# Optimization experiments

Hardware: AMD Instinct MI355X
Metric: run time of the kernel (lower is better)

## Reference

```python
import jax, jax.numpy as jnp
import numpy as np

T, B, D, H = 4096, 4, 1024, 8
EPS = 1e-5


def _ln(z, g, b):
    m = jnp.mean(z, axis=-1, keepdims=True)
    v = jnp.mean((z - m) ** 2, axis=-1, keepdims=True)
    return (z - m) * jax.lax.rsqrt(v + EPS) * g + b


def setup_inputs() -> dict:
    key = jax.random.key(0)
    ks = jax.random.split(key, 8)
    s = 0.02
    return {
        "x": jax.random.normal(ks[0], (T, B, D), dtype=jnp.float32),
        "norm_w": jnp.ones((D,), jnp.float32),
        "norm_b": jnp.zeros((D,), jnp.float32),
        "tnorm_w": jnp.ones((D,), jnp.float32),
        "tnorm_b": jnp.zeros((D,), jnp.float32),
        "Wq": jax.random.normal(ks[1], (D, D), jnp.float32) * s,
        "bq": jnp.zeros((D,), jnp.float32),
        "Wk": jax.random.normal(ks[2], (D, D), jnp.float32) * s,
        "bk": jnp.zeros((D,), jnp.float32),
        "Wv": jax.random.normal(ks[3], (D, D), jnp.float32) * s,
        "bv": jnp.zeros((D,), jnp.float32),
    }


def reference(x, norm_w, norm_b, tnorm_w, tnorm_b, Wq, bq, Wk, bk, Wv, bv):
    # x: (T, B, D) -> (B, T, D), matching torch x.permute(1, 0, 2)
    xb = jnp.transpose(x, (1, 0, 2))
    b, t, d = xb.shape
    hd = d // H
    xn = _ln(xb, norm_w, norm_b)          # query branch norm
    xtn = _ln(xb, tnorm_w, tnorm_b)       # key/value branch norm (text_norm applied to x)
    q = (xn @ Wq.T + bq).reshape(b, t, H, hd)
    k = (xtn @ Wk.T + bk).reshape(b, t, H, hd)
    v = (xtn @ Wv.T + bv).reshape(b, t, H, hd)
    q = jax.nn.softmax(q, axis=-1)        # softmax over head-dim
    k = jax.nn.softmax(k, axis=1)         # softmax over time
    # kv state: (B, H, hd, hd)
    att = jnp.einsum('bthd,bthl->bhdl', k, v)
    y = jnp.einsum('bthd,bhdl->bthl', q, att).reshape(b, t, d)
    return y  # original forward returns y directly (proj_out/dropout unused)
```

## Files before the change

kernel.cpp:

```cpp
#include <hip/hip_runtime.h>
#include <cstdint>

#define T_LEN 4096
#define BATCH 4
#define DIM   1024
#define NH    8
#define HDIM  128
#define ROWS  16384

typedef __bf16 bf16x8 __attribute__((ext_vector_type(8)));
typedef float  f32x4  __attribute__((ext_vector_type(4)));

__device__ __forceinline__ unsigned short f2bf(float f) {
  union { float f; unsigned u; } a; a.f = f;
  unsigned u = a.u;
  u += 0x7fff + ((u >> 16) & 1);
  return (unsigned short)(u >> 16);
}
__device__ __forceinline__ float bf2f(unsigned short h) {
  union { unsigned u; float f; } a; a.u = ((unsigned)h) << 16;
  return a.f;
}

__device__ __forceinline__ void gld_lds16(const unsigned short* g, unsigned short* l) {
  __builtin_amdgcn_global_load_lds(
      (const __attribute__((address_space(1))) unsigned int*)g,
      (__attribute__((address_space(3))) unsigned int*)l, 16, 0, 0);
}

__global__ __launch_bounds__(256) void ln_kernel(
    const float* __restrict__ x, const float* __restrict__ nw, const float* __restrict__ nb,
    const float* __restrict__ tw, const float* __restrict__ tb,
    unsigned short* __restrict__ xn, unsigned short* __restrict__ xtn) {
  int row = blockIdx.x;
  int t = row >> 2, b = row & 3;
  int tid = threadIdx.x;
  const float4 v = ((const float4*)(x + (size_t)row * DIM))[tid];
  float s  = v.x + v.y + v.z + v.w;
  float s2 = v.x*v.x + v.y*v.y + v.z*v.z + v.w*v.w;
#pragma unroll
  for (int o = 32; o; o >>= 1) { s += __shfl_xor(s, o); s2 += __shfl_xor(s2, o); }
  __shared__ float red[8];
  int wv = tid >> 6;
  if ((tid & 63) == 0) { red[wv] = s; red[4 + wv] = s2; }
  __syncthreads();
  s  = red[0] + red[1] + red[2] + red[3];
  s2 = red[4] + red[5] + red[6] + red[7];
  float mean = s * (1.0f / DIM);
  float var  = s2 * (1.0f / DIM) - mean * mean;
  float rstd = rsqrtf(var + 1e-5f);
  size_t orow = ((size_t)b * T_LEN + t) * DIM;
  int c0 = tid * 4;
  float xv[4] = {v.x, v.y, v.z, v.w};
  union { unsigned short u[4]; uint2 d; } o1, o2;
#pragma unroll
  for (int j = 0; j < 4; ++j) {
    int c = c0 + j;
    float xh = (xv[j] - mean) * rstd;
    o1.u[j] = f2bf(xh * nw[c] + nb[c]);
    o2.u[j] = f2bf(xh * tw[c] + tb[c]);
  }
  *(uint2*)(xn  + orow + c0) = o1.d;
  *(uint2*)(xtn + orow + c0) = o2.d;
}

__global__ __launch_bounds__(256) void wconv(
    const float* __restrict__ Wq, const float* __restrict__ Wk, const float* __restrict__ Wv,
    unsigned short* __restrict__ out) {
  int i4 = blockIdx.x * 256 + threadIdx.x;
  int w = i4 >> 18;
  const float* src = (w == 0) ? Wq : (w == 1 ? Wk : Wv);
  float4 v = ((const float4*)src)[i4 & 262143];
  union { unsigned short u[4]; uint2 d; } o;
  o.u[0] = f2bf(v.x); o.u[1] = f2bf(v.y); o.u[2] = f2bf(v.z); o.u[3] = f2bf(v.w);
  ((uint2*)out)[i4] = o.d;
}

template<int MODE>
__global__ __launch_bounds__(256) void qkv_gemm(
    const unsigned short* __restrict__ A, const unsigned short* __restrict__ W,
    const float* __restrict__ bias,
    unsigned short* __restrict__ outp, float* __restrict__ Zk) {
  int m0t = blockIdx.x * 128;
  int n0 = blockIdx.y * 128;
  __shared__ __align__(16) unsigned short smem[128 * 136];
  unsigned short* As = smem;
  unsigned short* Bs = smem + 8192;
  int tid = threadIdx.x;
  int wave = tid >> 6, lane = tid & 63;
  int wm = (wave >> 1) * 64, wn = (wave & 1) * 64;
  int l16 = lane & 15, kq = lane >> 4;
  int swz = l16 & 7;

  int srow = tid >> 3;
  int skk  = (((tid & 7) ^ ((tid >> 3) & 7)) * 8);
  const unsigned short* Ag = A + (size_t)(m0t + srow) * DIM + skk;
  const unsigned short* Wg = W + (size_t)(n0 + srow) * DIM + skk;
  unsigned short* Al = As + wave * 512;
  unsigned short* Bl = Bs + wave * 512;

  f32x4 acc[4][4] = {};

  for (int kt = 0; kt < DIM; kt += 64) {
#pragma unroll
    for (int p = 0; p < 4; ++p) {
      gld_lds16(Ag + (size_t)(p * 32) * DIM + kt, Al + p * 2048);
      gld_lds16(Wg + (size_t)(p * 32) * DIM + kt, Bl + p * 2048);
    }
    __syncthreads();
#pragma unroll
    for (int ks4 = 0; ks4 < 2; ++ks4) {
      int coff = (((kq + ks4 * 4) ^ swz) * 8);
      bf16x8 fa[4], fb[4];
#pragma unroll
      for (int i = 0; i < 4; ++i) {
        fa[i] = *(const bf16x8*)(As + (wm + i * 16 + l16) * 64 + coff);
        fb[i] = *(const bf16x8*)(Bs + (wn + i * 16 + l16) * 64 + coff);
      }
#pragma unroll
      for (int i = 0; i < 4; ++i)
#pragma unroll
        for (int j = 0; j < 4; ++j)
          acc[i][j] = __builtin_amdgcn_mfma_f32_16x16x32_bf16(fa[i], fb[j], acc[i][j], 0, 0, 0);
    }
    __syncthreads();
  }

  float bcol[4];
#pragma unroll
  for (int j = 0; j < 4; ++j) bcol[j] = bias[n0 + wn + j * 16 + l16];
#pragma unroll
  for (int i = 0; i < 4; ++i)
#pragma unroll
    for (int j = 0; j < 4; ++j)
#pragma unroll
      for (int r = 0; r < 4; ++r) acc[i][j][r] += bcol[j];

  if (MODE == 0) {
    float* redm = (float*)smem;
    float* reds = redm + 256;
#pragma unroll
    for (int i = 0; i < 4; ++i) {
#pragma unroll
      for (int r = 0; r < 4; ++r) {
        float pm = acc[i][0][r];
#pragma unroll
        for (int j = 1; j < 4; ++j) pm = fmaxf(pm, acc[i][j][r]);
        pm = fmaxf(pm, __shfl_xor(pm, 1));
        pm = fmaxf(pm, __shfl_xor(pm, 2));
        pm = fmaxf(pm, __shfl_xor(pm, 4));
        pm = fmaxf(pm, __shfl_xor(pm, 8));
        float ps = 0.0f;
#pragma unroll
        for (int j = 0; j < 4; ++j) ps += __expf(acc[i][j][r] - pm);
        ps += __shfl_xor(ps, 1);
        ps += __shfl_xor(ps, 2);
        ps += __shfl_xor(ps, 4);
        ps += __shfl_xor(ps, 8);
        if (l16 == 0) {
          int lrow = wm + i * 16 + kq * 4 + r;
          redm[lrow * 2 + (wave & 1)] = pm;
          reds[lrow * 2 + (wave & 1)] = ps;
        }
      }
    }
    __syncthreads();
#pragma unroll
    for (int i = 0; i < 4; ++i) {
#pragma unroll
      for (int r = 0; r < 4; ++r) {
        int lrow = wm + i * 16 + kq * 4 + r;
        float ma = redm[lrow * 2], mb = redm[lrow * 2 + 1];
        float sa = reds[lrow * 2], sb = reds[lrow * 2 + 1];
        float M = fmaxf(ma, mb);
        float inv = 1.0f / (sa * __expf(ma - M) + sb * __expf(mb - M));
        size_t gr = (size_t)(m0t + lrow) * DIM;
#pragma unroll
        for (int j = 0; j < 4; ++j) {
          int col = n0 + wn + j * 16 + l16;
          outp[gr + col] = f2bf(__expf(acc[i][j][r] - M) * inv);
        }
      }
    }
  } else {
    unsigned short* Ts = smem;
#pragma unroll
    for (int j = 0; j < 4; ++j) {
      int col = wn + j * 16 + l16;
#pragma unroll
      for (int i = 0; i < 4; ++i) {
        int t0 = wm + i * 16 + kq * 4;
        float v0 = acc[i][j][0], v1 = acc[i][j][1], v2 = acc[i][j][2], v3 = acc[i][j][3];
        if (MODE == 1) { v0 = __expf(v0); v1 = __expf(v1); v2 = __expf(v2); v3 = __expf(v3); }
        unsigned lo = (unsigned)f2bf(v0) | ((unsigned)f2bf(v1) << 16);
        unsigned hi = (unsigned)f2bf(v2) | ((unsigned)f2bf(v3) << 16);
        *(unsigned*)(Ts + col * 136 + t0)     = lo;
        *(unsigned*)(Ts + col * 136 + t0 + 2) = hi;
      }
    }
    __syncthreads();
    int col_o = tid >> 1;
    int th = (tid & 1) * 64;
    int b = m0t >> 12, tb = m0t & 4095;
    unsigned short* cp = outp + ((size_t)b * DIM + n0 + col_o) * T_LEN + tb + th;
    float zs = 0.0f;
#pragma unroll
    for (int c = 0; c < 8; ++c) {
      uint4 d = *(const uint4*)(Ts + col_o * 136 + th + c * 8);
      *(uint4*)(cp + c * 8) = d;
      if (MODE == 1) {
        const unsigned short* u = (const unsigned short*)&d;
#pragma unroll
        for (int e = 0; e < 8; ++e) zs += bf2f(u[e]);
      }
    }
    if (MODE == 1) {
      zs += __shfl_xor(zs, 1);
      if ((tid & 1) == 0) atomicAdd(&Zk[b * DIM + n0 + col_o], zs);
    }
  }
}

__global__ __launch_bounds__(256) void att_gemm(
    const unsigned short* __restrict__ vT, const unsigned short* __restrict__ ksmT,
    float* __restrict__ attT) {
  int kc = blockIdx.x;
  int bh = blockIdx.y;
  const unsigned short* Arow = vT   + (size_t)bh * HDIM * T_LEN;
  const unsigned short* Brow = ksmT + (size_t)bh * HDIM * T_LEN;
  __shared__ __align__(16) unsigned short As[128 * 64];
  __shared__ __align__(16) unsigned short Bs[128 * 64];
  int tid = threadIdx.x;
  int wave = tid >> 6, lane = tid & 63;
  int wm = (wave >> 1) * 64, wn = (wave & 1) * 64;
  int l16 = lane & 15, kq = lane >> 4;
  int swz = l16 & 7;
  int srow = tid >> 3;
  int skk = (((tid & 7) ^ ((tid >> 3) & 7)) * 8);
  const unsigned short* Ag = Arow + (size_t)srow * T_LEN + skk;
  const unsigned short* Bg = Brow + (size_t)srow * T_LEN + skk;
  unsigned short* Al = As + wave * 512;
  unsigned short* Bl = Bs + wave * 512;
  f32x4 acc[4][4] = {};
  int kbeg = kc * 256;
  for (int kt = kbeg; kt < kbeg + 256; kt += 64) {
#pragma unroll
    for (int p = 0; p < 4; ++p) {
      gld_lds16(Ag + (size_t)(p * 32) * T_LEN + kt, Al + p * 2048);
      gld_lds16(Bg + (size_t)(p * 32) * T_LEN + kt, Bl + p * 2048);
    }
    __syncthreads();
#pragma unroll
    for (int ks4 = 0; ks4 < 2; ++ks4) {
      int coff = (((kq + ks4 * 4) ^ swz) * 8);
      bf16x8 fa[4], fb[4];
#pragma unroll
      for (int i = 0; i < 4; ++i) {
        fa[i] = *(const bf16x8*)(As + (wm + i * 16 + l16) * 64 + coff);
        fb[i] = *(const bf16x8*)(Bs + (wn + i * 16 + l16) * 64 + coff);
      }
#pragma unroll
      for (int i = 0; i < 4; ++i)
#pragma unroll
        for (int j = 0; j < 4; ++j)
          acc[i][j] = __builtin_amdgcn_mfma_f32_16x16x32_bf16(fa[i], fb[j], acc[i][j], 0, 0, 0);
    }
    __syncthreads();
  }
#pragma unroll
  for (int j = 0; j < 4; ++j) {
    int col = wn + j * 16 + l16;
#pragma unroll
    for (int i = 0; i < 4; ++i) {
      int rb = wm + i * 16 + kq * 4;
#pragma unroll
      for (int r = 0; r < 4; ++r)
        atomicAdd(attT + (size_t)bh * 16384 + (size_t)(rb + r) * 128 + col, acc[i][j][r]);
    }
  }
}

__global__ __launch_bounds__(256) void attcvt(
    const float* __restrict__ attT, const float* __restrict__ Zk,
    unsigned short* __restrict__ attbf) {
  int idx = blockIdx.x * 256 + threadIdx.x;
  int bh = idx >> 14;
  int b = bh >> 3, h = bh & 7;
  int d = idx & 127;
  float z = Zk[b * DIM + h * HDIM + d];
  attbf[idx] = f2bf(attT[idx] / z);
}

__global__ __launch_bounds__(256) void y_gemm(
    const unsigned short* __restrict__ qsm, const unsigned short* __restrict__ attbf,
    float* __restrict__ out) {
  int h = blockIdx.y;
  int m0t = blockIdx.x * 128;
  int b = m0t >> 12;
  int bh = b * 8 + h;
  const unsigned short* Brow = attbf + (size_t)bh * 16384;
  __shared__ __align__(16) unsigned short As[128 * 64];
  __shared__ __align__(16) unsigned short Bs[128 * 64];
  int tid = threadIdx.x;
  int wave = tid >> 6, lane = tid & 63;
  int wm = (wave >> 1) * 64, wn = (wave & 1) * 64;
  int l16 = lane & 15, kq = lane >> 4;
  int swz = l16 & 7;
  int srow = tid >> 3;
  int skk = (((tid & 7) ^ ((tid >> 3) & 7)) * 8);
  const unsigned short* Ag = qsm + (size_t)(m0t + srow) * DIM + h * HDIM + skk;
  const unsigned short* Bg = Brow + (size_t)srow * HDIM + skk;
  unsigned short* Al = As + wave * 512;
  unsigned short* Bl = Bs + wave * 512;
  f32x4 acc[4][4] = {};
  for (int kt = 0; kt < HDIM; kt += 64) {
#pragma unroll
    for (int p = 0; p < 4; ++p) {
      gld_lds16(Ag + (size_t)(p * 32) * DIM + kt, Al + p * 2048);
      gld_lds16(Bg + (size_t)(p * 32) * HDIM + kt, Bl + p * 2048);
    }
    __syncthreads();
#pragma unroll
    for (int ks4 = 0; ks4 < 2; ++ks4) {
      int coff = (((kq + ks4 * 4) ^ swz) * 8);
      bf16x8 fa[4], fb[4];
#pragma unroll
      for (int i = 0; i < 4; ++i) {
        fa[i] = *(const bf16x8*)(As + (wm + i * 16 + l16) * 64 + coff);
        fb[i] = *(const bf16x8*)(Bs + (wn + i * 16 + l16) * 64 + coff);
      }
#pragma unroll
      for (int i = 0; i < 4; ++i)
#pragma unroll
        for (int j = 0; j < 4; ++j)
          acc[i][j] = __builtin_amdgcn_mfma_f32_16x16x32_bf16(fa[i], fb[j], acc[i][j], 0, 0, 0);
    }
    __syncthreads();
  }
#pragma unroll
  for (int j = 0; j < 4; ++j) {
    int col = wn + j * 16 + l16;
#pragma unroll
    for (int i = 0; i < 4; ++i) {
      int rb = wm + i * 16 + kq * 4;
#pragma unroll
      for (int r = 0; r < 4; ++r)
        out[(size_t)(m0t + rb + r) * DIM + h * HDIM + col] = acc[i][j][r];
    }
  }
}

extern "C" void kernel_launch(void* const* d_in, const int* in_sizes, int n_in,
                              void* d_out, int out_size, void* d_ws, size_t ws_size,
                              hipStream_t stream) {
  const float* x  = (const float*)d_in[0];
  const float* nw = (const float*)d_in[1];
  const float* nb = (const float*)d_in[2];
  const float* tw = (const float*)d_in[3];
  const float* tb = (const float*)d_in[4];
  const float* Wq = (const float*)d_in[5];
  const float* bq = (const float*)d_in[6];
  const float* Wk = (const float*)d_in[7];
  const float* bk = (const float*)d_in[8];
  const float* Wv = (const float*)d_in[9];
  const float* bv = (const float*)d_in[10];
  float* out = (float*)d_out;

  char* ws = (char*)d_ws;
  unsigned short* xn   = (unsigned short*)(ws);
  unsigned short* xtn  = (unsigned short*)(ws + 33554432);
  unsigned short* q    = (unsigned short*)(ws + 67108864);
  unsigned short* ksmT = (unsigned short*)(ws + 100663296);
  unsigned short* vT   = (unsigned short*)(ws + 134217728);
  unsigned short* wbf  = (unsigned short*)(ws + 167772160);
  float* attT          = (float*)(ws + 174063616);
  float* Zk            = (float*)(ws + 176160768);
  unsigned short* attbf= (unsigned short*)(ws + 176177152);

  (void)hipMemsetAsync(attT, 0, 32 * 128 * 128 * 4 + BATCH * DIM * 4, stream);
  ln_kernel<<<ROWS, 256, 0, stream>>>(x, nw, nb, tw, tb, xn, xtn);
  wconv<<<3072, 256, 0, stream>>>(Wq, Wk, Wv, wbf);
  qkv_gemm<1><<<dim3(128, 8), 256, 0, stream>>>(xtn, wbf + (size_t)1 * DIM * DIM, bk, ksmT, Zk);
  qkv_gemm<2><<<dim3(128, 8), 256, 0, stream>>>(xtn, wbf + (size_t)2 * DIM * DIM, bv, vT, Zk);
  qkv_gemm<0><<<dim3(128, 8), 256, 0, stream>>>(xn,  wbf,                         bq, q,  Zk);
  att_gemm<<<dim3(16, 32), 256, 0, stream>>>(vT, ksmT, attT);
  attcvt<<<2048, 256, 0, stream>>>(attT, Zk, attbf);
  y_gemm<<<dim3(128, 8), 256, 0, stream>>>(q, attbf, out);
}
```

Baseline: 358.6 us.

## Merge LN and weight conversion kernels, batch QKV GEMMs into one launch

```diff
diff --git a/kernel.cpp b/kernel.cpp
--- a/kernel.cpp
+++ b/kernel.cpp
@@ -28,62 +28,69 @@
       (__attribute__((address_space(3))) unsigned int*)l, 16, 0, 0);
 }
 
-__global__ __launch_bounds__(256) void ln_kernel(
+__global__ __launch_bounds__(256) void prep(
     const float* __restrict__ x, const float* __restrict__ nw, const float* __restrict__ nb,
     const float* __restrict__ tw, const float* __restrict__ tb,
-    unsigned short* __restrict__ xn, unsigned short* __restrict__ xtn) {
-  int row = blockIdx.x;
-  int t = row >> 2, b = row & 3;
+    unsigned short* __restrict__ xn, unsigned short* __restrict__ xtn,
+    const float* __restrict__ Wq, const float* __restrict__ Wk, const float* __restrict__ Wv,
+    unsigned short* __restrict__ wbf) {
   int tid = threadIdx.x;
-  const float4 v = ((const float4*)(x + (size_t)row * DIM))[tid];
-  float s  = v.x + v.y + v.z + v.w;
-  float s2 = v.x*v.x + v.y*v.y + v.z*v.z + v.w*v.w;
-#pragma unroll
-  for (int o = 32; o; o >>= 1) { s += __shfl_xor(s, o); s2 += __shfl_xor(s2, o); }
-  __shared__ float red[8];
-  int wv = tid >> 6;
-  if ((tid & 63) == 0) { red[wv] = s; red[4 + wv] = s2; }
-  __syncthreads();
-  s  = red[0] + red[1] + red[2] + red[3];
-  s2 = red[4] + red[5] + red[6] + red[7];
-  float mean = s * (1.0f / DIM);
-  float var  = s2 * (1.0f / DIM) - mean * mean;
-  float rstd = rsqrtf(var + 1e-5f);
-  size_t orow = ((size_t)b * T_LEN + t) * DIM;
-  int c0 = tid * 4;
-  float xv[4] = {v.x, v.y, v.z, v.w};
-  union { unsigned short u[4]; uint2 d; } o1, o2;
-#pragma unroll
-  for (int j = 0; j < 4; ++j) {
-    int c = c0 + j;
-    float xh = (xv[j] - mean) * rstd;
-    o1.u[j] = f2bf(xh * nw[c] + nb[c]);
-    o2.u[j] = f2bf(xh * tw[c] + tb[c]);
-  }
-  *(uint2*)(xn  + orow + c0) = o1.d;
-  *(uint2*)(xtn + orow + c0) = o2.d;
-}
-
-__global__ __launch_bounds__(256) void wconv(
-    const float* __restrict__ Wq, const float* __restrict__ Wk, const float* __restrict__ Wv,
-    unsigned short* __restrict__ out) {
-  int i4 = blockIdx.x * 256 + threadIdx.x;
-  int w = i4 >> 18;
-  const float* src = (w == 0) ? Wq : (w == 1 ? Wk : Wv);
-  float4 v = ((const float4*)src)[i4 & 262143];
-  union { unsigned short u[4]; uint2 d; } o;
-  o.u[0] = f2bf(v.x); o.u[1] = f2bf(v.y); o.u[2] = f2bf(v.z); o.u[3] = f2bf(v.w);
-  ((uint2*)out)[i4] = o.d;
-}
-
-template<int MODE>
+  if (blockIdx.x < ROWS) {
+    int row = blockIdx.x;
+    int t = row >> 2, b = row & 3;
+    const float4 v = ((const float4*)(x + (size_t)row * DIM))[tid];
+    float s  = v.x + v.y + v.z + v.w;
+    float s2 = v.x*v.x + v.y*v.y + v.z*v.z + v.w*v.w;
+#pragma unroll
+    for (int o = 32; o; o >>= 1) { s += __shfl_xor(s, o); s2 += __shfl_xor(s2, o); }
+    __shared__ float red[8];
+    int wv = tid >> 6;
+    if ((tid & 63) == 0) { red[wv] = s; red[4 + wv] = s2; }
+    __syncthreads();
+    s  = red[0] + red[1] + red[2] + red[3];
+    s2 = red[4] + red[5] + red[6] + red[7];
+    float mean = s * (1.0f / DIM);
+    float var  = s2 * (1.0f / DIM) - mean * mean;
+    float rstd = rsqrtf(var + 1e-5f);
+    size_t orow = ((size_t)b * T_LEN + t) * DIM;
+    int c0 = tid * 4;
+    float xv[4] = {v.x, v.y, v.z, v.w};
+    union { unsigned short u[4]; uint2 d; } o1, o2;
+#pragma unroll
+    for (int j = 0; j < 4; ++j) {
+      int c = c0 + j;
+      float xh = (xv[j] - mean) * rstd;
+      o1.u[j] = f2bf(xh * nw[c] + nb[c]);
+      o2.u[j] = f2bf(xh * tw[c] + tb[c]);
+    }
+    *(uint2*)(xn  + orow + c0) = o1.d;
+    *(uint2*)(xtn + orow + c0) = o2.d;
+  } else {
+    int i4 = (blockIdx.x - ROWS) * 256 + tid;
+    int w = i4 >> 18;
+    const float* src = (w == 0) ? Wq : (w == 1 ? Wk : Wv);
+    float4 v = ((const float4*)src)[i4 & 262143];
+    union { unsigned short u[4]; uint2 d; } o;
+    o.u[0] = f2bf(v.x); o.u[1] = f2bf(v.y); o.u[2] = f2bf(v.z); o.u[3] = f2bf(v.w);
+    ((uint2*)wbf)[i4] = o.d;
+  }
+}
+
 __global__ __launch_bounds__(256) void qkv_gemm(
-    const unsigned short* __restrict__ A, const unsigned short* __restrict__ W,
-    const float* __restrict__ bias,
-    unsigned short* __restrict__ outp, float* __restrict__ Zk) {
+    const unsigned short* __restrict__ xn, const unsigned short* __restrict__ xtn,
+    const unsigned short* __restrict__ wbf,
+    const float* __restrict__ bq, const float* __restrict__ bk, const float* __restrict__ bv,
+    unsigned short* __restrict__ qo, unsigned short* __restrict__ ko, unsigned short* __restrict__ vo,
+    float* __restrict__ Zk) {
+  int z = blockIdx.z;
+  const unsigned short* A = (z == 0) ? xn : xtn;
+  const unsigned short* W = wbf + (size_t)z * DIM * DIM;
+  const float* bias = (z == 0) ? bq : (z == 1 ? bk : bv);
+  unsigned short* outp = (z == 0) ? qo : (z == 1 ? ko : vo);
+
   int m0t = blockIdx.x * 128;
   int n0 = blockIdx.y * 128;
-  __shared__ __align__(16) unsigned short smem[128 * 136];
+  __shared__ __align__(16) unsigned short smem[16384];
   unsigned short* As = smem;
   unsigned short* Bs = smem + 8192;
   int tid = threadIdx.x;
@@ -136,7 +143,7 @@
 #pragma unroll
       for (int r = 0; r < 4; ++r) acc[i][j][r] += bcol[j];
 
-  if (MODE == 0) {
+  if (z == 0) {
     float* redm = (float*)smem;
     float* reds = redm + 256;
 #pragma unroll
@@ -184,37 +191,44 @@
     }
   } else {
     unsigned short* Ts = smem;
-#pragma unroll
-    for (int j = 0; j < 4; ++j) {
-      int col = wn + j * 16 + l16;
-#pragma unroll
-      for (int i = 0; i < 4; ++i) {
-        int t0 = wm + i * 16 + kq * 4;
-        float v0 = acc[i][j][0], v1 = acc[i][j][1], v2 = acc[i][j][2], v3 = acc[i][j][3];
-        if (MODE == 1) { v0 = __expf(v0); v1 = __expf(v1); v2 = __expf(v2); v3 = __expf(v3); }
-        unsigned lo = (unsigned)f2bf(v0) | ((unsigned)f2bf(v1) << 16);
-        unsigned hi = (unsigned)f2bf(v2) | ((unsigned)f2bf(v3) << 16);
-        *(unsigned*)(Ts + col * 136 + t0)     = lo;
-        *(unsigned*)(Ts + col * 136 + t0 + 2) = hi;
-      }
-    }
-    __syncthreads();
+    int b = m0t >> 12, tb = m0t & 4095;
+    bool doExp = (z == 1);
+    float zs = 0.0f;
     int col_o = tid >> 1;
-    int th = (tid & 1) * 64;
-    int b = m0t >> 12, tb = m0t & 4095;
-    unsigned short* cp = outp + ((size_t)b * DIM + n0 + col_o) * T_LEN + tb + th;
-    float zs = 0.0f;
-#pragma unroll
-    for (int c = 0; c < 8; ++c) {
-      uint4 d = *(const uint4*)(Ts + col_o * 136 + th + c * 8);
-      *(uint4*)(cp + c * 8) = d;
-      if (MODE == 1) {
-        const unsigned short* u = (const unsigned short*)&d;
-#pragma unroll
-        for (int e = 0; e < 8; ++e) zs += bf2f(u[e]);
-      }
-    }
-    if (MODE == 1) {
+    int th = (tid & 1) * 32;
+#pragma unroll
+    for (int p = 0; p < 2; ++p) {
+      __syncthreads();
+      if ((wm >> 6) == p) {
+#pragma unroll
+        for (int j = 0; j < 4; ++j) {
+          int col = wn + j * 16 + l16;
+#pragma unroll
+          for (int i = 0; i < 4; ++i) {
+            int tt = i * 16 + kq * 4;
+            float v0 = acc[i][j][0], v1 = acc[i][j][1], v2 = acc[i][j][2], v3 = acc[i][j][3];
+            if (doExp) { v0 = __expf(v0); v1 = __expf(v1); v2 = __expf(v2); v3 = __expf(v3); }
+            unsigned lo = (unsigned)f2bf(v0) | ((unsigned)f2bf(v1) << 16);
+            unsigned hi = (unsigned)f2bf(v2) | ((unsigned)f2bf(v3) << 16);
+            *(unsigned*)(Ts + col * 72 + tt)     = lo;
+            *(unsigned*)(Ts + col * 72 + tt + 2) = hi;
+          }
+        }
+      }
+      __syncthreads();
+      unsigned short* cp = outp + ((size_t)b * DIM + n0 + col_o) * T_LEN + tb + p * 64 + th;
+#pragma unroll
+      for (int c = 0; c < 4; ++c) {
+        uint4 d = *(const uint4*)(Ts + col_o * 72 + th + c * 8);
+        *(uint4*)(cp + c * 8) = d;
+        if (doExp) {
+          const unsigned short* u = (const unsigned short*)&d;
+#pragma unroll
+          for (int e = 0; e < 8; ++e) zs += bf2f(u[e]);
+        }
+      }
+    }
+    if (doExp) {
       zs += __shfl_xor(zs, 1);
       if ((tid & 1) == 0) atomicAdd(&Zk[b * DIM + n0 + col_o], zs);
     }
@@ -378,11 +392,8 @@
   unsigned short* attbf= (unsigned short*)(ws + 176177152);
 
   (void)hipMemsetAsync(attT, 0, 32 * 128 * 128 * 4 + BATCH * DIM * 4, stream);
-  ln_kernel<<<ROWS, 256, 0, stream>>>(x, nw, nb, tw, tb, xn, xtn);
-  wconv<<<3072, 256, 0, stream>>>(Wq, Wk, Wv, wbf);
-  qkv_gemm<1><<<dim3(128, 8), 256, 0, stream>>>(xtn, wbf + (size_t)1 * DIM * DIM, bk, ksmT, Zk);
-  qkv_gemm<2><<<dim3(128, 8), 256, 0, stream>>>(xtn, wbf + (size_t)2 * DIM * DIM, bv, vT, Zk);
-  qkv_gemm<0><<<dim3(128, 8), 256, 0, stream>>>(xn,  wbf,                         bq, q,  Zk);
+  prep<<<ROWS + 3072, 256, 0, stream>>>(x, nw, nb, tw, tb, xn, xtn, Wq, Wk, Wv, wbf);
+  qkv_gemm<<<dim3(128, 8, 3), 256, 0, stream>>>(xn, xtn, wbf, bq, bk, bv, q, ksmT, vT, Zk);
   att_gemm<<<dim3(16, 32), 256, 0, stream>>>(vT, ksmT, attT);
   attcvt<<<2048, 256, 0, stream>>>(attT, Zk, attbf);
   y_gemm<<<dim3(128, 8), 256, 0, stream>>>(q, attbf, out);
```

Result: faster. 343.8 us (-4.1%).
